# Optimization experiments

Hardware: AMD Instinct MI355X
Metric: run time of the kernel (lower is better)

## Reference

```python
import jax, jax.numpy as jnp
import numpy as np

S, N, CM, CZ, H, C = 256, 512, 256, 128, 8, 32
EPS = 1e-5


def layer_norm(x, gamma, beta):
    mu = jnp.mean(x, axis=-1, keepdims=True)
    var = jnp.var(x, axis=-1, keepdims=True)
    return (x - mu) * jax.lax.rsqrt(var + EPS) * gamma + beta


def setup_inputs() -> dict:
    key = jax.random.key(0)
    ks = jax.random.split(key, 10)
    sc = lambda fan_in: 1.0 / np.sqrt(fan_in)
    return {
        "msa_rep": jax.random.normal(ks[0], (S, N, CM), dtype=jnp.float32),
        "pair_rep": jax.random.normal(ks[1], (N, N, CZ), dtype=jnp.float32),
        "ln_msa_g": jnp.ones((CM,), jnp.float32),
        "ln_msa_b": jnp.zeros((CM,), jnp.float32),
        "Wv": jax.random.uniform(ks[2], (CM, H * C), jnp.float32, -sc(CM), sc(CM)),
        "bv": jax.random.uniform(ks[3], (H * C,), jnp.float32, -sc(CM), sc(CM)),
        "ln_z_g": jnp.ones((CZ,), jnp.float32),
        "ln_z_b": jnp.zeros((CZ,), jnp.float32),
        "Wb": jax.random.uniform(ks[4], (CZ, H), jnp.float32, -sc(CZ), sc(CZ)),
        "bb": jax.random.uniform(ks[5], (H,), jnp.float32, -sc(CZ), sc(CZ)),
        "Wg": jax.random.uniform(ks[6], (CM, H * C), jnp.float32, -sc(CM), sc(CM)),
        "bg": jax.random.uniform(ks[7], (H * C,), jnp.float32, -sc(CM), sc(CM)),
        "Wp": jax.random.uniform(ks[8], (H * C, CM), jnp.float32, -sc(H * C), sc(H * C)),
    }


def reference(msa_rep, pair_rep, ln_msa_g, ln_msa_b, Wv, bv, ln_z_g, ln_z_b, Wb, bb, Wg, bg, Wp):
    m = layer_norm(msa_rep, ln_msa_g, ln_msa_b)                 # [S,N,CM]
    v = (m @ Wv + bv).reshape(S, N, H, C)                       # [S,N,H,C]
    g = jax.nn.sigmoid(m @ Wg + bg).reshape(S, N, H, C)         # [S,N,H,C]
    b = layer_norm(pair_rep, ln_z_g, ln_z_b) @ Wb + bb          # [N,N,H]
    w = jax.nn.softmax(b, axis=-2)                              # softmax over key residue j
    # o[s,i,h,c] = sum_j w[i,j,h] * v[s,j,h,c]
    o = g * jnp.einsum('ijh,sjhc->sihc', w, v)                  # [S,N,H,C]
    return o.reshape(S, N, H * C) @ Wp                          # [S,N,CM]
```

## Files before the change

kernel.cpp:

```cpp
#include <hip/hip_runtime.h>
#include <hip/hip_bf16.h>
#include <math.h>

#define S 256
#define N 512
#define CM 256
#define CZ 128
#define H 8
#define C 32
#define HC 256

typedef __attribute__((ext_vector_type(8))) short short8v;
typedef __attribute__((ext_vector_type(4))) float f32x4;

#define GLOBAL_LOAD_LDS16(gsrc, ldst)                                          \
  __builtin_amdgcn_global_load_lds(                                            \
      (const __attribute__((address_space(1))) void*)(gsrc),                   \
      (__attribute__((address_space(3))) void*)(ldst), 16, 0, 0)

__global__ __launch_bounds__(256) void k_prep(
    const float* __restrict__ Wv, const float* __restrict__ Wg, const float* __restrict__ Wp,
    __hip_bfloat16* __restrict__ Wcat_t, __hip_bfloat16* __restrict__ Wp_t)
{
  const int k = blockIdx.x;
  const int n = threadIdx.x;
  Wcat_t[(size_t)n * CM + k]        = __float2bfloat16(Wv[(size_t)k * HC + n]);
  Wcat_t[(size_t)(n + HC) * CM + k] = __float2bfloat16(Wg[(size_t)k * HC + n]);
  Wp_t[(size_t)n * CM + k]          = __float2bfloat16(Wp[(size_t)k * CM + n]);
}

__global__ __launch_bounds__(256) void k_ln(
    const float* __restrict__ msa, const float* __restrict__ gamma, const float* __restrict__ beta,
    __hip_bfloat16* __restrict__ mbf)
{
  const int t = threadIdx.x, wav = t >> 6, lane = t & 63;
  const size_t row = (size_t)blockIdx.x * 4 + wav;
  const int k0 = lane * 4;
  const float4 xv = *(const float4*)(msa + row * CM + k0);
  float s  = xv.x + xv.y + xv.z + xv.w;
  float s2 = xv.x * xv.x + xv.y * xv.y + xv.z * xv.z + xv.w * xv.w;
#pragma unroll
  for (int off = 32; off > 0; off >>= 1) {
    s  += __shfl_xor(s, off);
    s2 += __shfl_xor(s2, off);
  }
  const float mu = s * (1.f / CM);
  const float rstd = rsqrtf(s2 * (1.f / CM) - mu * mu + 1e-5f);
  const float4 gm = *(const float4*)(gamma + k0);
  const float4 bt = *(const float4*)(beta + k0);
  union { __hip_bfloat16 b[4]; short4 v; } pk;
  pk.b[0] = __float2bfloat16((xv.x - mu) * rstd * gm.x + bt.x);
  pk.b[1] = __float2bfloat16((xv.y - mu) * rstd * gm.y + bt.y);
  pk.b[2] = __float2bfloat16((xv.z - mu) * rstd * gm.z + bt.z);
  pk.b[3] = __float2bfloat16((xv.w - mu) * rstd * gm.w + bt.w);
  *(short4*)(mbf + row * CM + k0) = pk.v;
}

__global__ __launch_bounds__(512) void k_mm1(
    const __hip_bfloat16* __restrict__ mbf, const __hip_bfloat16* __restrict__ Wcat_t,
    const float* __restrict__ bv, const float* __restrict__ bg,
    __hip_bfloat16* __restrict__ vc, __hip_bfloat16* __restrict__ gb)
{
  __shared__ __hip_bfloat16 Ac[8 * 256 * 8];
  __shared__ __hip_bfloat16 Bc[8 * 128 * 8];
  const int t = threadIdx.x;
  const int wave = t >> 6, lane = t & 63;
  const int wm = wave >> 1, wn = wave & 1;
  const int lr = lane & 15, lq = lane >> 4;
  const int n0 = blockIdx.x * 128;
  const int m0 = blockIdx.y * 256;
  const bool vhalf = (n0 < HC);

  float bias[4];
#pragma unroll
  for (int ni = 0; ni < 4; ++ni) {
    const int col = n0 + wn * 64 + ni * 16 + lr;
    bias[ni] = vhalf ? bv[col] : bg[col - HC];
  }
  f32x4 acc[4][4];
#pragma unroll
  for (int mi = 0; mi < 4; ++mi)
#pragma unroll
    for (int ni = 0; ni < 4; ++ni) acc[mi][ni] = (f32x4)bias[ni];

  for (int kt = 0; kt < CM / 64; ++kt) {
    __syncthreads();
#pragma unroll
    for (int u = 0; u < 4; ++u) {
      const int cc = wave * 4 + u;
      const int kb = cc & 7, ih = cc >> 3;
      GLOBAL_LOAD_LDS16(mbf + ((size_t)(m0 + ih * 64 + lane)) * CM + kt * 64 + kb * 8,
                        &Ac[(kb * 256 + ih * 64 + lane) * 8]);
    }
#pragma unroll
    for (int u = 0; u < 2; ++u) {
      const int cc = wave * 2 + u;
      const int kb = cc & 7, ih = cc >> 3;
      GLOBAL_LOAD_LDS16(Wcat_t + ((size_t)(n0 + ih * 64 + lane)) * CM + kt * 64 + kb * 8,
                        &Bc[(kb * 128 + ih * 64 + lane) * 8]);
    }
    __syncthreads();
#pragma unroll
    for (int kh = 0; kh < 2; ++kh) {
      const int ldb = lq + kh * 4;
      short8v a[4], b[4];
#pragma unroll
      for (int mi = 0; mi < 4; ++mi)
        a[mi] = *(const short8v*)&Ac[((ldb * 256) + wm * 64 + mi * 16 + lr) * 8];
#pragma unroll
      for (int ni = 0; ni < 4; ++ni)
        b[ni] = *(const short8v*)&Bc[((ldb * 128) + wn * 64 + ni * 16 + lr) * 8];
#pragma unroll
      for (int mi = 0; mi < 4; ++mi)
#pragma unroll
        for (int ni = 0; ni < 4; ++ni)
          acc[mi][ni] = __builtin_amdgcn_mfma_f32_16x16x32_bf16(a[mi], b[ni], acc[mi][ni], 0, 0, 0);
    }
  }

  if (vhalf) {
#pragma unroll
    for (int mi = 0; mi < 4; ++mi) {
      const int rowb = m0 + wm * 64 + mi * 16 + lq * 4;
      const int s = rowb >> 9;
      const int j = rowb & (N - 1);
      const int jb = j >> 3, jlo = (lq & 1) * 4;
#pragma unroll
      for (int ni = 0; ni < 4; ++ni) {
        const int col = n0 + wn * 64 + ni * 16 + lr;
        const int h = col >> 5, c = col & 31;
        union { __hip_bfloat16 b[4]; short4 v; } pk;
#pragma unroll
        for (int r = 0; r < 4; ++r) pk.b[r] = __float2bfloat16(acc[mi][ni][r]);
        *(short4*)(vc + ((size_t)(h * (N / 8) + jb) * (S * C) + s * C + c) * 8 + jlo) = pk.v;
      }
    }
  } else {
#pragma unroll
    for (int mi = 0; mi < 4; ++mi) {
      const int rowb = m0 + wm * 64 + mi * 16 + lq * 4;
#pragma unroll
      for (int ni = 0; ni < 4; ++ni) {
        const int colp = (n0 - HC) + wn * 64 + ni * 16 + lr;
#pragma unroll
        for (int r = 0; r < 4; ++r)
          gb[(size_t)(rowb + r) * HC + colp] =
              __float2bfloat16(1.f / (1.f + __expf(-acc[mi][ni][r])));
      }
    }
  }
}

__global__ __launch_bounds__(256) void k_lnb_sm(
    const float* __restrict__ pair, const float* __restrict__ gamma, const float* __restrict__ beta,
    const float* __restrict__ Wb, __hip_bfloat16* __restrict__ wbh)
{
  __shared__ float slog[H][N];
  const int t = threadIdx.x, wav = t >> 6, lane = t & 63;
  const int q = lane & 15, sub = lane >> 4;
  const int k0 = q * 8;
  const size_t i = blockIdx.x;

  float wreg[8][8];
#pragma unroll
  for (int kk = 0; kk < 8; ++kk) {
    *(float4*)&wreg[kk][0] = *(const float4*)&Wb[(k0 + kk) * H];
    *(float4*)&wreg[kk][4] = *(const float4*)&Wb[(k0 + kk) * H + 4];
  }
  const float4 gm0 = *(const float4*)(gamma + k0);
  const float4 gm1 = *(const float4*)(gamma + k0 + 4);
  const float4 bt0 = *(const float4*)(beta + k0);
  const float4 bt1 = *(const float4*)(beta + k0 + 4);

#pragma unroll 2
  for (int it = 0; it < 32; ++it) {
    const int j = it * 16 + wav * 4 + sub;
    const float* x = pair + (i * N + j) * CZ + k0;
    const float4 x0 = *(const float4*)(x);
    const float4 x1 = *(const float4*)(x + 4);

    float s  = x0.x + x0.y + x0.z + x0.w + x1.x + x1.y + x1.z + x1.w;
    float s2 = x0.x * x0.x + x0.y * x0.y + x0.z * x0.z + x0.w * x0.w
             + x1.x * x1.x + x1.y * x1.y + x1.z * x1.z + x1.w * x1.w;
#pragma unroll
    for (int off = 8; off > 0; off >>= 1) {
      s  += __shfl_xor(s, off);
      s2 += __shfl_xor(s2, off);
    }
    const float mu = s * (1.f / CZ);
    const float rstd = rsqrtf(s2 * (1.f / CZ) - mu * mu + 1e-5f);

    float xn[8];
    xn[0] = (x0.x - mu) * rstd * gm0.x + bt0.x;
    xn[1] = (x0.y - mu) * rstd * gm0.y + bt0.y;
    xn[2] = (x0.z - mu) * rstd * gm0.z + bt0.z;
    xn[3] = (x0.w - mu) * rstd * gm0.w + bt0.w;
    xn[4] = (x1.x - mu) * rstd * gm1.x + bt1.x;
    xn[5] = (x1.y - mu) * rstd * gm1.y + bt1.y;
    xn[6] = (x1.z - mu) * rstd * gm1.z + bt1.z;
    xn[7] = (x1.w - mu) * rstd * gm1.w + bt1.w;

    float acc[8];
#pragma unroll
    for (int h = 0; h < 8; ++h) acc[h] = 0.f;
#pragma unroll
    for (int kk = 0; kk < 8; ++kk)
#pragma unroll
      for (int h = 0; h < 8; ++h) acc[h] += xn[kk] * wreg[kk][h];

#pragma unroll
    for (int h = 0; h < 8; ++h) {
#pragma unroll
      for (int off = 8; off > 0; off >>= 1) acc[h] += __shfl_xor(acc[h], off);
    }
    if (q == 0) {
#pragma unroll
      for (int h = 0; h < 8; ++h) slog[h][j] = acc[h];
    }
  }
  __syncthreads();

#pragma unroll
  for (int hh2 = 0; hh2 < 2; ++hh2) {
    const int hh = wav * 2 + hh2;
    const int j0 = lane * 8;
    const float4 p0 = *(const float4*)&slog[hh][j0];
    const float4 p1 = *(const float4*)&slog[hh][j0 + 4];
    float mx = fmaxf(fmaxf(fmaxf(p0.x, p0.y), fmaxf(p0.z, p0.w)),
                     fmaxf(fmaxf(p1.x, p1.y), fmaxf(p1.z, p1.w)));
#pragma unroll
    for (int off = 32; off > 0; off >>= 1) mx = fmaxf(mx, __shfl_xor(mx, off));
    float e[8];
    e[0] = __expf(p0.x - mx); e[1] = __expf(p0.y - mx);
    e[2] = __expf(p0.z - mx); e[3] = __expf(p0.w - mx);
    e[4] = __expf(p1.x - mx); e[5] = __expf(p1.y - mx);
    e[6] = __expf(p1.z - mx); e[7] = __expf(p1.w - mx);
    float sum = ((e[0] + e[1]) + (e[2] + e[3])) + ((e[4] + e[5]) + (e[6] + e[7]));
#pragma unroll
    for (int off = 32; off > 0; off >>= 1) sum += __shfl_xor(sum, off);
    const float inv = 1.f / sum;
    union { __hip_bfloat16 b[8]; short8v v; } pk;
#pragma unroll
    for (int r = 0; r < 8; ++r) pk.b[r] = __float2bfloat16(e[r] * inv);
    *(short8v*)(wbh + ((size_t)hh * N + i) * N + j0) = pk.v;
  }
}

__global__ __launch_bounds__(512) void k_attn_mfma(
    const __hip_bfloat16* __restrict__ vc, const __hip_bfloat16* __restrict__ wbh,
    __hip_bfloat16* gb)
{
  __shared__ __hip_bfloat16 Ac[8 * 256 * 8];
  __shared__ __hip_bfloat16 Bc[8 * 128 * 8];

  const int t = threadIdx.x;
  const int wave = t >> 6, lane = t & 63;
  const int wm = wave >> 1, wn = wave & 1;
  const int lr = lane & 15, lq = lane >> 4;
  const int n0 = blockIdx.x * 128;
  const int i0 = blockIdx.y * 256;
  const int h  = blockIdx.z;

  f32x4 acc[4][4];
#pragma unroll
  for (int mi = 0; mi < 4; ++mi)
#pragma unroll
    for (int ni = 0; ni < 4; ++ni) acc[mi][ni] = (f32x4)0.f;

  const __hip_bfloat16* Abase = wbh + ((size_t)h * N + i0) * N;
  const __hip_bfloat16* Bbase = vc + (size_t)h * (N / 8) * (S * C) * 8 + (size_t)n0 * 8;

  for (int kt = 0; kt < N / 64; ++kt) {
    __syncthreads();
#pragma unroll
    for (int u = 0; u < 4; ++u) {
      const int cc = wave * 4 + u;
      const int kb = cc & 7, ih = cc >> 3;
      GLOBAL_LOAD_LDS16(Abase + ((size_t)(ih * 64 + lane)) * N + kt * 64 + kb * 8,
                        &Ac[(kb * 256 + ih * 64 + lane) * 8]);
    }
#pragma unroll
    for (int u = 0; u < 2; ++u) {
      const int cc = wave * 2 + u;
      const int kb = cc & 7, ih = cc >> 3;
      GLOBAL_LOAD_LDS16(Bbase + ((size_t)(kt * 8 + kb) * (S * C) + ih * 64 + lane) * 8,
                        &Bc[(kb * 128 + ih * 64 + lane) * 8]);
    }
    __syncthreads();

#pragma unroll
    for (int kh = 0; kh < 2; ++kh) {
      const int ldb = lq + kh * 4;
      short8v a[4], b[4];
#pragma unroll
      for (int mi = 0; mi < 4; ++mi)
        a[mi] = *(const short8v*)&Ac[((ldb * 256) + wm * 64 + mi * 16 + lr) * 8];
#pragma unroll
      for (int ni = 0; ni < 4; ++ni)
        b[ni] = *(const short8v*)&Bc[((ldb * 128) + wn * 64 + ni * 16 + lr) * 8];
#pragma unroll
      for (int mi = 0; mi < 4; ++mi)
#pragma unroll
        for (int ni = 0; ni < 4; ++ni)
          acc[mi][ni] = __builtin_amdgcn_mfma_f32_16x16x32_bf16(a[mi], b[ni], acc[mi][ni], 0, 0, 0);
    }
  }

#pragma unroll
  for (int mi = 0; mi < 4; ++mi)
#pragma unroll
    for (int ni = 0; ni < 4; ++ni) {
      const int n = n0 + wn * 64 + ni * 16 + lr;
      const int sidx = n >> 5, c = n & 31;
#pragma unroll
      for (int r = 0; r < 4; ++r) {
        const int i = i0 + wm * 64 + mi * 16 + lq * 4 + r;
        const size_t idx = (((size_t)sidx * N + i) << 8) + h * C + c;
        const float gv = __bfloat162float(gb[idx]);
        gb[idx] = __float2bfloat16(gv * acc[mi][ni][r]);
      }
    }
}

__global__ __launch_bounds__(512) void k_out_mfma(
    const __hip_bfloat16* __restrict__ ogb, const __hip_bfloat16* __restrict__ Wp_t,
    float* __restrict__ out)
{
  __shared__ __hip_bfloat16 Ac[8 * 256 * 8];
  __shared__ __hip_bfloat16 Bc[8 * 128 * 8];
  const int t = threadIdx.x;
  const int wave = t >> 6, lane = t & 63;
  const int wm = wave >> 1, wn = wave & 1;
  const int lr = lane & 15, lq = lane >> 4;
  const int n0 = blockIdx.x * 128;
  const int m0 = blockIdx.y * 256;

  f32x4 acc[4][4];
#pragma unroll
  for (int mi = 0; mi < 4; ++mi)
#pragma unroll
    for (int ni = 0; ni < 4; ++ni) acc[mi][ni] = (f32x4)0.f;

  for (int kt = 0; kt < CM / 64; ++kt) {
    __syncthreads();
#pragma unroll
    for (int u = 0; u < 4; ++u) {
      const int cc = wave * 4 + u;
      const int kb = cc & 7, ih = cc >> 3;
      GLOBAL_LOAD_LDS16(ogb + ((size_t)(m0 + ih * 64 + lane)) * CM + kt * 64 + kb * 8,
                        &Ac[(kb * 256 + ih * 64 + lane) * 8]);
    }
#pragma unroll
    for (int u = 0; u < 2; ++u) {
      const int cc = wave * 2 + u;
      const int kb = cc & 7, ih = cc >> 3;
      GLOBAL_LOAD_LDS16(Wp_t + ((size_t)(n0 + ih * 64 + lane)) * CM + kt * 64 + kb * 8,
                        &Bc[(kb * 128 + ih * 64 + lane) * 8]);
    }
    __syncthreads();
#pragma unroll
    for (int kh = 0; kh < 2; ++kh) {
      const int ldb = lq + kh * 4;
      short8v a[4], b[4];
#pragma unroll
      for (int mi = 0; mi < 4; ++mi)
        a[mi] = *(const short8v*)&Ac[((ldb * 256) + wm * 64 + mi * 16 + lr) * 8];
#pragma unroll
      for (int ni = 0; ni < 4; ++ni)
        b[ni] = *(const short8v*)&Bc[((ldb * 128) + wn * 64 + ni * 16 + lr) * 8];
#pragma unroll
      for (int mi = 0; mi < 4; ++mi)
#pragma unroll
        for (int ni = 0; ni < 4; ++ni)
          acc[mi][ni] = __builtin_amdgcn_mfma_f32_16x16x32_bf16(a[mi], b[ni], acc[mi][ni], 0, 0, 0);
    }
  }

#pragma unroll
  for (int mi = 0; mi < 4; ++mi) {
    const int rowb = m0 + wm * 64 + mi * 16 + lq * 4;
#pragma unroll
    for (int ni = 0; ni < 4; ++ni) {
      const int col = n0 + wn * 64 + ni * 16 + lr;
#pragma unroll
      for (int r = 0; r < 4; ++r)
        out[(size_t)(rowb + r) * CM + col] = acc[mi][ni][r];
    }
  }
}

extern "C" void kernel_launch(void* const* d_in, const int* in_sizes, int n_in,
                              void* d_out, int out_size, void* d_ws, size_t ws_size,
                              hipStream_t stream)
{
  const float* msa      = (const float*)d_in[0];
  const float* pair     = (const float*)d_in[1];
  const float* ln_msa_g = (const float*)d_in[2];
  const float* ln_msa_b = (const float*)d_in[3];
  const float* Wv       = (const float*)d_in[4];
  const float* bv       = (const float*)d_in[5];
  const float* ln_z_g   = (const float*)d_in[6];
  const float* ln_z_b   = (const float*)d_in[7];
  const float* Wb       = (const float*)d_in[8];
  const float* bb       = (const float*)d_in[9];
  const float* Wg       = (const float*)d_in[10];
  const float* bg       = (const float*)d_in[11];
  const float* Wp       = (const float*)d_in[12];
  float* out = (float*)d_out;
  (void)bb;

  char* w = (char*)d_ws;
  __hip_bfloat16* vc     = (__hip_bfloat16*)(w);
  __hip_bfloat16* mbf    = (__hip_bfloat16*)(w + 67108864);
  __hip_bfloat16* gb     = (__hip_bfloat16*)(w + 134217728);
  __hip_bfloat16* wbh    = (__hip_bfloat16*)(w + 209715200);
  __hip_bfloat16* Wcat_t = (__hip_bfloat16*)(w + 213909504);
  __hip_bfloat16* Wp_t   = (__hip_bfloat16*)(w + 214171648);

  k_prep<<<256, 256, 0, stream>>>(Wv, Wg, Wp, Wcat_t, Wp_t);
  k_ln<<<S * N / 4, 256, 0, stream>>>(msa, ln_msa_g, ln_msa_b, mbf);
  dim3 g1(4, S * N / 256);
  k_mm1<<<g1, 512, 0, stream>>>(mbf, Wcat_t, bv, bg, vc, gb);
  k_lnb_sm<<<N, 256, 0, stream>>>(pair, ln_z_g, ln_z_b, Wb, wbh);
  dim3 g4(S * C / 128, N / 256, H);
  k_attn_mfma<<<g4, 512, 0, stream>>>(vc, wbh, gb);
  dim3 g5(2, S * N / 256);
  k_out_mfma<<<g5, 512, 0, stream>>>(gb, Wp_t, out);
}
```

Before: 329.5 us.

## Fuse MSA layernorm apply into first GEMM and remap block order for XCD locality

Replaces the standalone layernorm kernel, which wrote a bf16 normalized copy of msa, with a small per-row stats kernel. The first GEMM now reads fp32 msa directly and normalizes and converts it while staging its A tile into LDS. This removes a full bf16 intermediate write and re-read, but each of the 4 N-tiles reloads the fp32 rows, and the async global-to-LDS copy for A becomes synchronous register loads. It also flattens grids and remaps block IDs with a stride of 8, so blocks sharing data land on the same XCD and share its L2.

```diff
diff --git a/kernel.cpp b/kernel.cpp
--- a/kernel.cpp
+++ b/kernel.cpp
@@ -29,35 +29,36 @@
   Wp_t[(size_t)n * CM + k]          = __float2bfloat16(Wp[(size_t)k * CM + n]);
 }
 
-__global__ __launch_bounds__(256) void k_ln(
-    const float* __restrict__ msa, const float* __restrict__ gamma, const float* __restrict__ beta,
-    __hip_bfloat16* __restrict__ mbf)
-{
-  const int t = threadIdx.x, wav = t >> 6, lane = t & 63;
-  const size_t row = (size_t)blockIdx.x * 4 + wav;
-  const int k0 = lane * 4;
-  const float4 xv = *(const float4*)(msa + row * CM + k0);
-  float s  = xv.x + xv.y + xv.z + xv.w;
-  float s2 = xv.x * xv.x + xv.y * xv.y + xv.z * xv.z + xv.w * xv.w;
-#pragma unroll
-  for (int off = 32; off > 0; off >>= 1) {
+__global__ __launch_bounds__(256) void k_stats(
+    const float* __restrict__ msa, float2* __restrict__ stats)
+{
+  const int t = threadIdx.x;
+  const int q = t & 15;
+  const size_t row = (size_t)blockIdx.x * 16 + (t >> 4);
+  const float* x = msa + row * CM + q * 16;
+  float s = 0.f, s2 = 0.f;
+#pragma unroll
+  for (int u = 0; u < 4; ++u) {
+    const float4 xv = *(const float4*)(x + u * 4);
+    s  += xv.x + xv.y + xv.z + xv.w;
+    s2 += xv.x * xv.x + xv.y * xv.y + xv.z * xv.z + xv.w * xv.w;
+  }
+#pragma unroll
+  for (int off = 8; off > 0; off >>= 1) {
     s  += __shfl_xor(s, off);
     s2 += __shfl_xor(s2, off);
   }
-  const float mu = s * (1.f / CM);
-  const float rstd = rsqrtf(s2 * (1.f / CM) - mu * mu + 1e-5f);
-  const float4 gm = *(const float4*)(gamma + k0);
-  const float4 bt = *(const float4*)(beta + k0);
-  union { __hip_bfloat16 b[4]; short4 v; } pk;
-  pk.b[0] = __float2bfloat16((xv.x - mu) * rstd * gm.x + bt.x);
-  pk.b[1] = __float2bfloat16((xv.y - mu) * rstd * gm.y + bt.y);
-  pk.b[2] = __float2bfloat16((xv.z - mu) * rstd * gm.z + bt.z);
-  pk.b[3] = __float2bfloat16((xv.w - mu) * rstd * gm.w + bt.w);
-  *(short4*)(mbf + row * CM + k0) = pk.v;
-}
-
-__global__ __launch_bounds__(512) void k_mm1(
-    const __hip_bfloat16* __restrict__ mbf, const __hip_bfloat16* __restrict__ Wcat_t,
+  if (q == 0) {
+    const float mu = s * (1.f / CM);
+    const float rstd = rsqrtf(s2 * (1.f / CM) - mu * mu + 1e-5f);
+    stats[row] = make_float2(mu, rstd);
+  }
+}
+
+__global__ __launch_bounds__(512) void k_mm1f(
+    const float* __restrict__ msa, const float2* __restrict__ stats,
+    const float* __restrict__ gamma, const float* __restrict__ beta,
+    const __hip_bfloat16* __restrict__ Wcat_t,
     const float* __restrict__ bv, const float* __restrict__ bg,
     __hip_bfloat16* __restrict__ vc, __hip_bfloat16* __restrict__ gb)
 {
@@ -67,9 +68,16 @@
   const int wave = t >> 6, lane = t & 63;
   const int wm = wave >> 1, wn = wave & 1;
   const int lr = lane & 15, lq = lane >> 4;
-  const int n0 = blockIdx.x * 128;
-  const int m0 = blockIdx.y * 256;
+  const int bid = blockIdx.x;
+  const int virt = (bid & 7) * 256 + (bid >> 3);
+  const int n0 = (virt & 3) * 128;
+  const int m0 = (virt >> 2) * 256;
   const bool vhalf = (n0 < HC);
+
+  const int arow = t & 255;
+  const int kbh  = t >> 8;
+  const float2 st = stats[m0 + arow];
+  const float* msarow = msa + (size_t)(m0 + arow) * CM;
 
   float bias[4];
 #pragma unroll
@@ -85,12 +93,26 @@
 
   for (int kt = 0; kt < CM / 64; ++kt) {
     __syncthreads();
-#pragma unroll
+#pragma unroll 2
     for (int u = 0; u < 4; ++u) {
-      const int cc = wave * 4 + u;
-      const int kb = cc & 7, ih = cc >> 3;
-      GLOBAL_LOAD_LDS16(mbf + ((size_t)(m0 + ih * 64 + lane)) * CM + kt * 64 + kb * 8,
-                        &Ac[(kb * 256 + ih * 64 + lane) * 8]);
+      const int kb = u * 2 + kbh;
+      const int gc = kt * 64 + kb * 8;
+      const float4 x0 = *(const float4*)(msarow + gc);
+      const float4 x1 = *(const float4*)(msarow + gc + 4);
+      const float4 g0 = *(const float4*)(gamma + gc);
+      const float4 g1 = *(const float4*)(gamma + gc + 4);
+      const float4 b0 = *(const float4*)(beta + gc);
+      const float4 b1 = *(const float4*)(beta + gc + 4);
+      union { __hip_bfloat16 b[8]; short8v v; } pk;
+      pk.b[0] = __float2bfloat16((x0.x - st.x) * st.y * g0.x + b0.x);
+      pk.b[1] = __float2bfloat16((x0.y - st.x) * st.y * g0.y + b0.y);
+      pk.b[2] = __float2bfloat16((x0.z - st.x) * st.y * g0.z + b0.z);
+      pk.b[3] = __float2bfloat16((x0.w - st.x) * st.y * g0.w + b0.w);
+      pk.b[4] = __float2bfloat16((x1.x - st.x) * st.y * g1.x + b1.x);
+      pk.b[5] = __float2bfloat16((x1.y - st.x) * st.y * g1.y + b1.y);
+      pk.b[6] = __float2bfloat16((x1.z - st.x) * st.y * g1.z + b1.z);
+      pk.b[7] = __float2bfloat16((x1.w - st.x) * st.y * g1.w + b1.w);
+      *(short8v*)&Ac[(kb * 256 + arow) * 8] = pk.v;
     }
 #pragma unroll
     for (int u = 0; u < 2; ++u) {
@@ -257,9 +279,12 @@
   const int wave = t >> 6, lane = t & 63;
   const int wm = wave >> 1, wn = wave & 1;
   const int lr = lane & 15, lq = lane >> 4;
-  const int n0 = blockIdx.x * 128;
-  const int i0 = blockIdx.y * 256;
-  const int h  = blockIdx.z;
+  const int bid = blockIdx.x;
+  const int virt = (bid & 7) * 128 + (bid >> 3);
+  const int h  = virt >> 7;
+  const int w_ = virt & 127;
+  const int i0 = (w_ >> 6) * 256;
+  const int n0 = (w_ & 63) * 128;
 
   f32x4 acc[4][4];
 #pragma unroll
@@ -332,8 +357,10 @@
   const int wave = t >> 6, lane = t & 63;
   const int wm = wave >> 1, wn = wave & 1;
   const int lr = lane & 15, lq = lane >> 4;
-  const int n0 = blockIdx.x * 128;
-  const int m0 = blockIdx.y * 256;
+  const int bid = blockIdx.x;
+  const int virt = (bid & 7) * 128 + (bid >> 3);
+  const int n0 = (virt & 1) * 128;
+  const int m0 = (virt >> 1) * 256;
 
   f32x4 acc[4][4];
 #pragma unroll
@@ -411,19 +438,16 @@
 
   char* w = (char*)d_ws;
   __hip_bfloat16* vc     = (__hip_bfloat16*)(w);
-  __hip_bfloat16* mbf    = (__hip_bfloat16*)(w + 67108864);
+  float2*         stats  = (float2*)        (w + 67108864);
   __hip_bfloat16* gb     = (__hip_bfloat16*)(w + 134217728);
   __hip_bfloat16* wbh    = (__hip_bfloat16*)(w + 209715200);
   __hip_bfloat16* Wcat_t = (__hip_bfloat16*)(w + 213909504);
   __hip_bfloat16* Wp_t   = (__hip_bfloat16*)(w + 214171648);
 
   k_prep<<<256, 256, 0, stream>>>(Wv, Wg, Wp, Wcat_t, Wp_t);
-  k_ln<<<S * N / 4, 256, 0, stream>>>(msa, ln_msa_g, ln_msa_b, mbf);
-  dim3 g1(4, S * N / 256);
-  k_mm1<<<g1, 512, 0, stream>>>(mbf, Wcat_t, bv, bg, vc, gb);
+  k_stats<<<S * N / 16, 256, 0, stream>>>(msa, stats);
+  k_mm1f<<<2048, 512, 0, stream>>>(msa, stats, ln_msa_g, ln_msa_b, Wcat_t, bv, bg, vc, gb);
   k_lnb_sm<<<N, 256, 0, stream>>>(pair, ln_z_g, ln_z_b, Wb, wbh);
-  dim3 g4(S * C / 128, N / 256, H);
-  k_attn_mfma<<<g4, 512, 0, stream>>>(vc, wbh, gb);
-  dim3 g5(2, S * N / 256);
-  k_out_mfma<<<g5, 512, 0, stream>>>(gb, Wp_t, out);
-}
+  k_attn_mfma<<<1024, 512, 0, stream>>>(vc, wbh, gb);
+  k_out_mfma<<<1024, 512, 0, stream>>>(gb, Wp_t, out);
+}
```

Result: slower. 386.1 us (+17.2%).
